# Kernel optimization log

Measured on AMD Instinct MI355X. Metric: run time of the kernel, lower is better.

Reference implementation:

```python
import jax, jax.numpy as jnp
import numpy as np

T = 5          # Newton-Schulz iterations
EPS = 1e-05


def reference(X):
    # X: (B, C, L); training-mode IterNorm whitening with num_groups=1
    B, C, L = X.shape
    x = jnp.transpose(X, (1, 0, 2)).reshape(C, -1)        # (d, m)
    d, m = x.shape
    mean = jnp.mean(x, axis=-1, keepdims=True)
    xc = x - mean                                         # (d, m)
    I = jnp.eye(d, dtype=X.dtype)
    Sigma = I * EPS + (xc @ xc.T) * (1.0 / m)             # (d, d)
    rTr = 1.0 / jnp.trace(Sigma)                          # scalar
    Sigma_N = Sigma * rTr
    P = I
    for _ in range(T):
        P = 1.5 * P - 0.5 * (P @ P @ P) @ Sigma_N
    wm = P * jnp.sqrt(rTr)                                # whitening matrix
    xn = wm @ xc                                          # (d, m)
    Xn = jnp.transpose(xn.reshape(C, B, L), (1, 0, 2))
    return Xn


def setup_inputs() -> dict:
    key = jax.random.key(0)
    X = jax.random.normal(key, (32, 64, 8192), dtype=jnp.float32)
    return {"X": X}
```

## Files before the change

### kernel.cpp

```cpp
#include <hip/hip_runtime.h>
#include <math.h>

#define L_DIM   8192
#define NCH     64
#define M_TOT_F 262144.0f
#define EPS_F   1e-5f
#define GTPB    4
#define ATPB    4
#define PSTRIDE 4224

typedef float f32x4 __attribute__((ext_vector_type(4)));
typedef short bf16x8 __attribute__((ext_vector_type(8)));

union U8 { unsigned u[4]; bf16x8 v; };

__device__ __forceinline__ void cvt2(float f0, float f1, unsigned& h, unsigned& l) {
    unsigned u0 = __float_as_uint(f0), u1 = __float_as_uint(f1);
    h = (u0 >> 16) | (u1 & 0xFFFF0000u);
    float r0 = f0 - __uint_as_float(u0 & 0xFFFF0000u);
    float r1 = f1 - __uint_as_float(u1 & 0xFFFF0000u);
    l = (__float_as_uint(r0) >> 16) | (__float_as_uint(r1) & 0xFFFF0000u);
}

__device__ __forceinline__ void split16(float v, unsigned short& h, unsigned short& l) {
    unsigned u = __float_as_uint(v);
    h = (unsigned short)(u >> 16);
    float r = v - __uint_as_float(u & 0xFFFF0000u);
    l = (unsigned short)(__float_as_uint(r) >> 16);
}

__device__ __forceinline__ f32x4 mfma16(bf16x8 a, bf16x8 b, f32x4 c) {
    return __builtin_amdgcn_mfma_f32_16x16x32_bf16(a, b, c, 0, 0, 0);
}

__device__ __forceinline__ f32x4 fzero() {
    f32x4 z; z[0] = 0.f; z[1] = 0.f; z[2] = 0.f; z[3] = 0.f; return z;
}

__global__ __launch_bounds__(256) void gram_kernel(const float* __restrict__ X,
                                                   float* __restrict__ P) {
    __shared__ __align__(16) unsigned char arena[32768];
    unsigned short (*hfrag)[4096] = (unsigned short(*)[4096])(arena);
    unsigned short (*lfrag)[4096] = (unsigned short(*)[4096])(arena + 16384);
    float* fg2 = (float*)arena;

    const int tid  = threadIdx.x;
    const int w    = tid >> 6;
    const int lane = tid & 63;
    const int m    = lane & 15;
    const int q    = lane >> 4;
    const int row  = 16 * w + m;

    f32x4 acc1[4], acc2[4];
#pragma unroll
    for (int nb = 0; nb < 4; ++nb) { acc1[nb] = fzero(); acc2[nb] = fzero(); }
    float sacc = 0.f;

    const int tile0 = blockIdx.x * GTPB;
    float4 v[GTPB][4];
#pragma unroll
    for (int t = 0; t < GTPB; ++t) {
        int tt = tile0 + t;
        const float* src = X + ((size_t)((tt >> 7) * NCH + row)) * L_DIM + ((tt & 127) << 6) + 8 * q;
        v[t][0] = *(const float4*)(src);
        v[t][1] = *(const float4*)(src + 4);
        v[t][2] = *(const float4*)(src + 32);
        v[t][3] = *(const float4*)(src + 36);
    }

#pragma unroll
    for (int t = 0; t < GTPB; ++t) {
        const int p = t & 1;
#pragma unroll
        for (int i = 0; i < 4; ++i) sacc += v[t][i].x + v[t][i].y + v[t][i].z + v[t][i].w;

        bf16x8 Ah[2], Al[2];
#pragma unroll
        for (int k = 0; k < 2; ++k) {
            U8 H, L;
            cvt2(v[t][2 * k].x,     v[t][2 * k].y,     H.u[0], L.u[0]);
            cvt2(v[t][2 * k].z,     v[t][2 * k].w,     H.u[1], L.u[1]);
            cvt2(v[t][2 * k + 1].x, v[t][2 * k + 1].y, H.u[2], L.u[2]);
            cvt2(v[t][2 * k + 1].z, v[t][2 * k + 1].w, H.u[3], L.u[3]);
            Ah[k] = H.v; Al[k] = L.v;
            int chunk = ((w * 2 + k) * 4 + q) * 16 + m;
            *(bf16x8*)&hfrag[p][chunk * 8] = H.v;
            *(bf16x8*)&lfrag[p][chunk * 8] = L.v;
        }
        __syncthreads();

#pragma unroll
        for (int k = 0; k < 2; ++k)
#pragma unroll
            for (int nb = 0; nb < 4; ++nb) {
                int chunk = ((nb * 2 + k) * 4 + q) * 16 + m;
                bf16x8 bh = *(const bf16x8*)&hfrag[p][chunk * 8];
                bf16x8 bl = *(const bf16x8*)&lfrag[p][chunk * 8];
                acc1[nb] = mfma16(Ah[k], bh, acc1[nb]);
                acc2[nb] = mfma16(Ah[k], bl, acc2[nb]);
            }
    }

    __syncthreads();
#pragma unroll
    for (int nb = 0; nb < 4; ++nb)
#pragma unroll
        for (int r = 0; r < 4; ++r) {
            int grow = 16 * w + 4 * q + r;
            int gcol = 16 * nb + m;
            fg2[grow * 65 + gcol] = acc2[nb][r];
        }
    __syncthreads();

    float* base = P + (size_t)blockIdx.x * PSTRIDE;
#pragma unroll
    for (int nb = 0; nb < 4; ++nb)
#pragma unroll
        for (int r = 0; r < 4; ++r) {
            int grow = 16 * w + 4 * q + r;
            int gcol = 16 * nb + m;
            base[grow * 64 + gcol] = acc1[nb][r] + acc2[nb][r] + fg2[gcol * 65 + grow];
        }
    sacc += __shfl_xor(sacc, 16);
    sacc += __shfl_xor(sacc, 32);
    if (q == 0) base[4096 + row] = sacc;
}

__global__ __launch_bounds__(256) void reduce_kernel(const float* __restrict__ P,
                                                     float* __restrict__ H0,
                                                     float* __restrict__ H1) {
    const int tid = threadIdx.x;
    const int w = tid >> 6, lane = tid & 63;
    const int s = blockIdx.x % 65;
    const int h = blockIdx.x / 65;
    const int e0 = s * 64;
    const float* base = P + (size_t)(h * 512 + w * 128) * PSTRIDE + e0 + lane;
    float a0 = 0.f, a1 = 0.f, a2 = 0.f, a3 = 0.f;
#pragma unroll 8
    for (int i = 0; i < 32; ++i) {
        const float* p = base + (size_t)(4 * i) * PSTRIDE;
        a0 += p[0];
        a1 += p[PSTRIDE];
        a2 += p[2 * PSTRIDE];
        a3 += p[3 * PSTRIDE];
    }
    float a = (a0 + a1) + (a2 + a3);
    __shared__ float red[4][64];
    red[w][lane] = a;
    __syncthreads();
    if (w == 0) {
        float r = red[0][lane] + red[1][lane] + red[2][lane] + red[3][lane];
        (h ? H1 : H0)[e0 + lane] = r;
    }
}

__device__ __forceinline__ void mm_core8(f32x4* acc,
                                         const unsigned short* Xh, const unsigned short* Xl,
                                         const unsigned short* Yh, const unsigned short* Yl,
                                         int rg, int nbb, int m, int q) {
#pragma unroll
    for (int k0 = 0; k0 < 64; k0 += 32) {
        bf16x8 xh = *(const bf16x8*)&Xh[(16 * rg + m) * 72 + k0 + 8 * q];
        bf16x8 xl = *(const bf16x8*)&Xl[(16 * rg + m) * 72 + k0 + 8 * q];
#pragma unroll
        for (int j = 0; j < 2; ++j) {
            int nb = nbb + j;
            bf16x8 yh = *(const bf16x8*)&Yh[(16 * nb + m) * 72 + k0 + 8 * q];
            bf16x8 yl = *(const bf16x8*)&Yl[(16 * nb + m) * 72 + k0 + 8 * q];
            acc[j] = mfma16(xh, yh, acc[j]);
            acc[j] = mfma16(xh, yl, acc[j]);
            acc[j] = mfma16(xl, yh, acc[j]);
        }
    }
}

__device__ __forceinline__ void mm_pl8(unsigned short* Dh, unsigned short* Dl,
                                       const unsigned short* Xh, const unsigned short* Xl,
                                       const unsigned short* Yh, const unsigned short* Yl,
                                       int rg, int nbb, int m, int q) {
    f32x4 acc[2];
    acc[0] = fzero(); acc[1] = fzero();
    mm_core8(acc, Xh, Xl, Yh, Yl, rg, nbb, m, q);
#pragma unroll
    for (int j = 0; j < 2; ++j)
#pragma unroll
        for (int r = 0; r < 4; ++r) {
            int row = 16 * rg + 4 * q + r, col = 16 * (nbb + j) + m;
            unsigned short h, l;
            split16(acc[j][r], h, l);
            Dh[row * 72 + col] = h;
            Dl[row * 72 + col] = l;
        }
}

__global__ __launch_bounds__(512) void ns_kernel(float* __restrict__ ws,
                                                 const float* __restrict__ H1) {
    __shared__ __align__(16) float Pf[64 * 68];
    __shared__ __align__(16) unsigned short Ph[64 * 72], Pl[64 * 72];
    __shared__ __align__(16) unsigned short Sh[64 * 72], Sl[64 * 72];
    __shared__ __align__(16) unsigned short T1h[64 * 72], T1l[64 * 72];
    __shared__ __align__(16) unsigned short T2h[64 * 72], T2l[64 * 72];
    __shared__ float mu[64];
    __shared__ float scal[2];

    const int tid = threadIdx.x;
    const int w8 = tid >> 6, lane = tid & 63;
    const int m = lane & 15, q = lane >> 4;
    const int rg = w8 >> 1, nbb = (w8 & 1) << 1;
    const float inv_m = 1.0f / M_TOT_F;

    if (tid < 64) mu[tid] = (ws[4096 + tid] + H1[4096 + tid]) * inv_m;
    __syncthreads();

    if (tid < 64) {
        int e = tid * 65;
        float g  = (ws[e] + H1[e]) * inv_m;
        float sd = g - mu[tid] * mu[tid] + EPS_F;
#pragma unroll
        for (int off = 32; off >= 1; off >>= 1) sd += __shfl_xor(sd, off);
        if (tid == 0) { scal[0] = 1.0f / sd; scal[1] = sqrtf(1.0f / sd); }
    }
    __syncthreads();
    const float rTr = scal[0];

    for (int e = tid; e < 4096; e += 512) {
        int i = e >> 6, j = e & 63;
        float g   = (ws[e] + H1[e]) * inv_m;
        float sig = g - mu[i] * mu[j] + ((i == j) ? EPS_F : 0.f);
        float sn  = sig * rTr;
        unsigned short h, l;
        split16(sn, h, l);
        Sh[i * 72 + j] = h; Sl[i * 72 + j] = l;
        float pv = ((i == j) ? 1.5f : 0.f) - 0.5f * sn;
        Pf[i * 68 + j] = pv;
        split16(pv, h, l);
        Ph[i * 72 + j] = h; Pl[i * 72 + j] = l;
    }
    __syncthreads();

    for (int it = 0; it < 4; ++it) {
        mm_pl8(T1h, T1l, Ph, Pl, Ph, Pl, rg, nbb, m, q);
        __syncthreads();
        mm_pl8(T2h, T2l, T1h, T1l, Ph, Pl, rg, nbb, m, q);
        __syncthreads();
        f32x4 acc[2];
        acc[0] = fzero(); acc[1] = fzero();
        mm_core8(acc, T2h, T2l, Sh, Sl, rg, nbb, m, q);
#pragma unroll
        for (int j = 0; j < 2; ++j)
#pragma unroll
            for (int r = 0; r < 4; ++r) {
                int row = 16 * rg + 4 * q + r, col = 16 * (nbb + j) + m;
                int idx = row * 68 + col;
                float pv = 1.5f * Pf[idx] - 0.5f * acc[j][r];
                Pf[idx] = pv;
                unsigned short h, l;
                split16(pv, h, l);
                Ph[row * 72 + col] = h;
                Pl[row * 72 + col] = l;
            }
        __syncthreads();
    }

    const float s = scal[1];
    unsigned short* hp = (unsigned short*)ws;
    unsigned short* lp = hp + 4096;
    for (int e = tid; e < 4096; e += 512) {
        int i = e >> 6, j = e & 63;
        float v = Pf[i * 68 + j] * s;
        unsigned short h, l;
        split16(v, h, l);
        hp[e] = h;
        lp[e] = l;
    }
    if (tid < 64) {
        float a = 0.f;
#pragma unroll 8
        for (int k = 0; k < 64; ++k) a += Pf[tid * 68 + k] * mu[k];
        ws[8256 + tid] = -a * s;
    }
}

__global__ __launch_bounds__(256) void apply_kernel(const float* __restrict__ X,
                                                    float* __restrict__ Y,
                                                    const float* __restrict__ ws) {
    __shared__ __align__(16) unsigned short hplane[2][4096];
    __shared__ __align__(16) unsigned short lplane[2][4096];
    const int tid  = threadIdx.x;
    const int w    = tid >> 6;
    const int lane = tid & 63;
    const int m    = lane & 15;
    const int q    = lane >> 4;
    const int cp   = tid & 31;
    const int lg   = tid >> 5;

    const unsigned short* hp = (const unsigned short*)ws;
    const unsigned short* lp = hp + 4096;
    bf16x8 Ah[2], Al[2];
#pragma unroll
    for (int kk = 0; kk < 2; ++kk) {
        Ah[kk] = *(const bf16x8*)&hp[(16 * w + m) * 64 + 32 * kk + 8 * q];
        Al[kk] = *(const bf16x8*)&lp[(16 * w + m) * 64 + 32 * kk + 8 * q];
    }
    const float4 bias4 = *(const float4*)&ws[8256 + 16 * w + 4 * q];

    float4 va[ATPB][2], vb[ATPB][2];
#pragma unroll
    for (int t = 0; t < ATPB; ++t) {
        int tile = blockIdx.x * ATPB + t;
        const float* xb = X + (size_t)(tile >> 7) * (NCH * L_DIM) + ((tile & 127) << 6)
                          + (size_t)(2 * cp) * L_DIM + 4 * lg;
#pragma unroll
        for (int ss = 0; ss < 2; ++ss) {
            va[t][ss] = *(const float4*)(xb + 32 * ss);
            vb[t][ss] = *(const float4*)(xb + 32 * ss + L_DIM);
        }
    }

#pragma unroll
    for (int t = 0; t < ATPB; ++t) {
        int tile = blockIdx.x * ATPB + t;
        int bidx = tile >> 7;
        int l0   = (tile & 127) << 6;
        const int p = t & 1;
        unsigned* hw2 = (unsigned*)hplane[p];
        unsigned* lw2 = (unsigned*)lplane[p];

#pragma unroll
        for (int ss = 0; ss < 2; ++ss) {
            float fa[4], fb[4];
            *(float4*)fa = va[t][ss];
            *(float4*)fb = vb[t][ss];
#pragma unroll
            for (int i = 0; i < 4; ++i) {
                int l = 4 * lg + 32 * ss + i;
                unsigned h, lo2;
                cvt2(fa[i], fb[i], h, lo2);
                int widx = l * 32 + (((cp >> 2) ^ (l & 7)) << 2) + (cp & 3);
                hw2[widx] = h;
                lw2[widx] = lo2;
            }
        }
        __syncthreads();

        f32x4 acc[4];
#pragma unroll
        for (int nb = 0; nb < 4; ++nb) {
            acc[nb][0] = bias4.x; acc[nb][1] = bias4.y;
            acc[nb][2] = bias4.z; acc[nb][3] = bias4.w;
        }
#pragma unroll
        for (int kk = 0; kk < 2; ++kk)
#pragma unroll
            for (int nb = 0; nb < 4; ++nb) {
                int l = 16 * nb + m;
                int saddr = l * 64 + ((((4 * kk + q) ^ (l & 7))) << 3);
                bf16x8 bh = *(const bf16x8*)&hplane[p][saddr];
                bf16x8 bl = *(const bf16x8*)&lplane[p][saddr];
                acc[nb] = mfma16(Ah[kk], bh, acc[nb]);
                acc[nb] = mfma16(Ah[kk], bl, acc[nb]);
                acc[nb] = mfma16(Al[kk], bh, acc[nb]);
            }

#pragma unroll
        for (int nb = 0; nb < 4; ++nb)
#pragma unroll
            for (int rr = 0; rr < 4; ++rr)
                Y[((size_t)bidx * NCH + 16 * w + 4 * q + rr) * L_DIM + l0 + 16 * nb + m] = acc[nb][rr];
    }
}

extern "C" void kernel_launch(void* const* d_in, const int* in_sizes, int n_in,
                              void* d_out, int out_size, void* d_ws, size_t ws_size,
                              hipStream_t stream) {
    const float* X = (const float*)d_in[0];
    float* Y  = (float*)d_out;
    float* ws = (float*)d_ws;
    float* scratch = (float*)d_out;
    float* H1 = scratch + (size_t)1024 * PSTRIDE;

    hipLaunchKernelGGL(gram_kernel,   dim3(1024), dim3(256), 0, stream, X, scratch);
    hipLaunchKernelGGL(reduce_kernel, dim3(130),  dim3(256), 0, stream, scratch, ws, H1);
    hipLaunchKernelGGL(ns_kernel,     dim3(1),    dim3(512), 0, stream, ws, H1);
    hipLaunchKernelGGL(apply_kernel,  dim3(1024), dim3(256), 0, stream, X, Y, ws);
}
```

Before: 147.0 us.

## Fuse partial-Gram reduction with Newton-Schulz via last-block-done election

Merges the reduce kernel and the single-block Newton-Schulz kernel into one launch. Each of 130 blocks reduces its slice of the partial Gram buffers and writes it to workspace with atomic stores. A global atomic counter then elects the last finishing block to run the Newton-Schulz iterations, reading the reduced sums through agent-scope atomic loads. This removes one kernel launch and its gap, at the cost of a global counter and fences, and the elected block starts only after all others finish.

```diff
diff --git a/kernel.cpp b/kernel.cpp
--- a/kernel.cpp
+++ b/kernel.cpp
@@ -8,11 +8,15 @@
 #define GTPB    4
 #define ATPB    4
 #define PSTRIDE 4224
+#define WSH     8448
+#define HSTR    4224
 
 typedef float f32x4 __attribute__((ext_vector_type(4)));
 typedef short bf16x8 __attribute__((ext_vector_type(8)));
 
 union U8 { unsigned u[4]; bf16x8 v; };
+
+__device__ unsigned rns_count;
 
 __device__ __forceinline__ void cvt2(float f0, float f1, unsigned& h, unsigned& l) {
     unsigned u0 = __float_as_uint(f0), u1 = __float_as_uint(f1);
@@ -27,6 +31,10 @@
     h = (unsigned short)(u >> 16);
     float r = v - __uint_as_float(u & 0xFFFF0000u);
     l = (unsigned short)(__float_as_uint(r) >> 16);
+}
+
+__device__ __forceinline__ float aload(const float* p) {
+    return __hip_atomic_load(p, __ATOMIC_RELAXED, __HIP_MEMORY_SCOPE_AGENT);
 }
 
 __device__ __forceinline__ f32x4 mfma16(bf16x8 a, bf16x8 b, f32x4 c) {
@@ -126,34 +134,6 @@
     if (q == 0) base[4096 + row] = sacc;
 }
 
-__global__ __launch_bounds__(256) void reduce_kernel(const float* __restrict__ P,
-                                                     float* __restrict__ H0,
-                                                     float* __restrict__ H1) {
-    const int tid = threadIdx.x;
-    const int w = tid >> 6, lane = tid & 63;
-    const int s = blockIdx.x % 65;
-    const int h = blockIdx.x / 65;
-    const int e0 = s * 64;
-    const float* base = P + (size_t)(h * 512 + w * 128) * PSTRIDE + e0 + lane;
-    float a0 = 0.f, a1 = 0.f, a2 = 0.f, a3 = 0.f;
-#pragma unroll 8
-    for (int i = 0; i < 32; ++i) {
-        const float* p = base + (size_t)(4 * i) * PSTRIDE;
-        a0 += p[0];
-        a1 += p[PSTRIDE];
-        a2 += p[2 * PSTRIDE];
-        a3 += p[3 * PSTRIDE];
-    }
-    float a = (a0 + a1) + (a2 + a3);
-    __shared__ float red[4][64];
-    red[w][lane] = a;
-    __syncthreads();
-    if (w == 0) {
-        float r = red[0][lane] + red[1][lane] + red[2][lane] + red[3][lane];
-        (h ? H1 : H0)[e0 + lane] = r;
-    }
-}
-
 __device__ __forceinline__ void mm_core8(f32x4* acc,
                                          const unsigned short* Xh, const unsigned short* Xl,
                                          const unsigned short* Yh, const unsigned short* Yl,
@@ -193,8 +173,8 @@
         }
 }
 
-__global__ __launch_bounds__(512) void ns_kernel(float* __restrict__ ws,
-                                                 const float* __restrict__ H1) {
+__global__ __launch_bounds__(512) void reduce_ns_kernel(const float* __restrict__ P,
+                                                        float* __restrict__ ws) {
     __shared__ __align__(16) float Pf[64 * 68];
     __shared__ __align__(16) unsigned short Ph[64 * 72], Pl[64 * 72];
     __shared__ __align__(16) unsigned short Sh[64 * 72], Sl[64 * 72];
@@ -202,6 +182,8 @@
     __shared__ __align__(16) unsigned short T2h[64 * 72], T2l[64 * 72];
     __shared__ float mu[64];
     __shared__ float scal[2];
+    __shared__ float red[8][64];
+    __shared__ unsigned elect;
 
     const int tid = threadIdx.x;
     const int w8 = tid >> 6, lane = tid & 63;
@@ -209,12 +191,48 @@
     const int rg = w8 >> 1, nbb = (w8 & 1) << 1;
     const float inv_m = 1.0f / M_TOT_F;
 
-    if (tid < 64) mu[tid] = (ws[4096 + tid] + H1[4096 + tid]) * inv_m;
+    {
+        const int s = blockIdx.x % 65;
+        const int h = blockIdx.x / 65;
+        const int e0 = s * 64;
+        const float* base = P + (size_t)(h * 512 + w8 * 64) * PSTRIDE + e0 + lane;
+        float a0 = 0.f, a1 = 0.f, a2 = 0.f, a3 = 0.f;
+#pragma unroll 4
+        for (int i = 0; i < 16; ++i) {
+            const float* p = base + (size_t)(4 * i) * PSTRIDE;
+            a0 += p[0];
+            a1 += p[PSTRIDE];
+            a2 += p[2 * PSTRIDE];
+            a3 += p[3 * PSTRIDE];
+        }
+        red[w8][lane] = (a0 + a1) + (a2 + a3);
+        __syncthreads();
+        if (w8 == 0) {
+            float r = ((red[0][lane] + red[1][lane]) + (red[2][lane] + red[3][lane]))
+                    + ((red[4][lane] + red[5][lane]) + (red[6][lane] + red[7][lane]));
+            __hip_atomic_store(&ws[WSH + h * HSTR + e0 + lane], r,
+                               __ATOMIC_RELAXED, __HIP_MEMORY_SCOPE_AGENT);
+        }
+    }
+    __syncthreads();
+    if (tid == 0) {
+        __threadfence();
+        unsigned o = __hip_atomic_fetch_add(&rns_count, 1u, __ATOMIC_ACQ_REL,
+                                            __HIP_MEMORY_SCOPE_AGENT);
+        elect = (o == 129) ? 1u : 0u;
+        if (o == 129)
+            __hip_atomic_store(&rns_count, 0u, __ATOMIC_RELAXED, __HIP_MEMORY_SCOPE_AGENT);
+    }
+    __syncthreads();
+    if (!elect) return;
+    __threadfence();
+
+    if (tid < 64) mu[tid] = (aload(&ws[WSH + 4096 + tid]) + aload(&ws[WSH + HSTR + 4096 + tid])) * inv_m;
     __syncthreads();
 
     if (tid < 64) {
         int e = tid * 65;
-        float g  = (ws[e] + H1[e]) * inv_m;
+        float g  = (aload(&ws[WSH + e]) + aload(&ws[WSH + HSTR + e])) * inv_m;
         float sd = g - mu[tid] * mu[tid] + EPS_F;
 #pragma unroll
         for (int off = 32; off >= 1; off >>= 1) sd += __shfl_xor(sd, off);
@@ -225,7 +243,7 @@
 
     for (int e = tid; e < 4096; e += 512) {
         int i = e >> 6, j = e & 63;
-        float g   = (ws[e] + H1[e]) * inv_m;
+        float g   = (aload(&ws[WSH + e]) + aload(&ws[WSH + HSTR + e])) * inv_m;
         float sig = g - mu[i] * mu[j] + ((i == j) ? EPS_F : 0.f);
         float sn  = sig * rTr;
         unsigned short h, l;
@@ -377,10 +395,8 @@
     float* Y  = (float*)d_out;
     float* ws = (float*)d_ws;
     float* scratch = (float*)d_out;
-    float* H1 = scratch + (size_t)1024 * PSTRIDE;
-
-    hipLaunchKernelGGL(gram_kernel,   dim3(1024), dim3(256), 0, stream, X, scratch);
-    hipLaunchKernelGGL(reduce_kernel, dim3(130),  dim3(256), 0, stream, scratch, ws, H1);
-    hipLaunchKernelGGL(ns_kernel,     dim3(1),    dim3(512), 0, stream, ws, H1);
-    hipLaunchKernelGGL(apply_kernel,  dim3(1024), dim3(256), 0, stream, X, Y, ws);
-}
+
+    hipLaunchKernelGGL(gram_kernel,      dim3(1024), dim3(256), 0, stream, X, scratch);
+    hipLaunchKernelGGL(reduce_ns_kernel, dim3(130),  dim3(512), 0, stream, scratch, ws);
+    hipLaunchKernelGGL(apply_kernel,     dim3(1024), dim3(256), 0, stream, X, Y, ws);
+}
```

Measured after the change: 150.6 us. 1.02x slower.

## Stream gram tile loads through 3-slot ring, widen NS kernel to 16 waves

Applied to the files above, without the earlier changes.

The gram kernel now keeps only three tiles of loaded input in registers and issues the fourth tile's load after the first tile is converted, instead of loading all four up front. Together with a min-blocks-per-CU launch bound on the gram and apply kernels, this lowers register pressure so more blocks can be resident. The single-block Newton-Schulz kernel moves from 8 to 16 waves, each computing one 16x16 output tile instead of two, to shorten the serial critical path of that one block. The risks are that the register cap forces spills, and that the smaller per-wave work in the NS kernel leaves more of its time in synchronisation.

```diff
diff --git a/kernel.cpp b/kernel.cpp
--- a/kernel.cpp
+++ b/kernel.cpp
@@ -37,8 +37,8 @@
     f32x4 z; z[0] = 0.f; z[1] = 0.f; z[2] = 0.f; z[3] = 0.f; return z;
 }
 
-__global__ __launch_bounds__(256) void gram_kernel(const float* __restrict__ X,
-                                                   float* __restrict__ P) {
+__global__ __launch_bounds__(256, 4) void gram_kernel(const float* __restrict__ X,
+                                                      float* __restrict__ P) {
     __shared__ __align__(16) unsigned char arena[32768];
     unsigned short (*hfrag)[4096] = (unsigned short(*)[4096])(arena);
     unsigned short (*lfrag)[4096] = (unsigned short(*)[4096])(arena + 16384);
@@ -57,36 +57,43 @@
     float sacc = 0.f;
 
     const int tile0 = blockIdx.x * GTPB;
-    float4 v[GTPB][4];
+    float4 v[3][4];
+
+#define LDT(slot, tt)  {                                                                   \
+        const float* src_ = X + ((size_t)(((tt) >> 7) * NCH + row)) * L_DIM                \
+                              + (((tt) & 127) << 6) + 8 * q;                               \
+        v[slot][0] = *(const float4*)(src_);                                               \
+        v[slot][1] = *(const float4*)(src_ + 4);                                           \
+        v[slot][2] = *(const float4*)(src_ + 32);                                          \
+        v[slot][3] = *(const float4*)(src_ + 36);                                          \
+    }
+
+#pragma unroll
+    for (int t = 0; t < 3; ++t) LDT(t, tile0 + t)
+
 #pragma unroll
     for (int t = 0; t < GTPB; ++t) {
-        int tt = tile0 + t;
-        const float* src = X + ((size_t)((tt >> 7) * NCH + row)) * L_DIM + ((tt & 127) << 6) + 8 * q;
-        v[t][0] = *(const float4*)(src);
-        v[t][1] = *(const float4*)(src + 4);
-        v[t][2] = *(const float4*)(src + 32);
-        v[t][3] = *(const float4*)(src + 36);
-    }
-
-#pragma unroll
-    for (int t = 0; t < GTPB; ++t) {
-        const int p = t & 1;
-#pragma unroll
-        for (int i = 0; i < 4; ++i) sacc += v[t][i].x + v[t][i].y + v[t][i].z + v[t][i].w;
+        const int slot = t % 3;
+        const int p    = t & 1;
+#pragma unroll
+        for (int i = 0; i < 4; ++i)
+            sacc += v[slot][i].x + v[slot][i].y + v[slot][i].z + v[slot][i].w;
 
         bf16x8 Ah[2], Al[2];
 #pragma unroll
         for (int k = 0; k < 2; ++k) {
             U8 H, L;
-            cvt2(v[t][2 * k].x,     v[t][2 * k].y,     H.u[0], L.u[0]);
-            cvt2(v[t][2 * k].z,     v[t][2 * k].w,     H.u[1], L.u[1]);
-            cvt2(v[t][2 * k + 1].x, v[t][2 * k + 1].y, H.u[2], L.u[2]);
-            cvt2(v[t][2 * k + 1].z, v[t][2 * k + 1].w, H.u[3], L.u[3]);
+            cvt2(v[slot][2 * k].x,     v[slot][2 * k].y,     H.u[0], L.u[0]);
+            cvt2(v[slot][2 * k].z,     v[slot][2 * k].w,     H.u[1], L.u[1]);
+            cvt2(v[slot][2 * k + 1].x, v[slot][2 * k + 1].y, H.u[2], L.u[2]);
+            cvt2(v[slot][2 * k + 1].z, v[slot][2 * k + 1].w, H.u[3], L.u[3]);
             Ah[k] = H.v; Al[k] = L.v;
             int chunk = ((w * 2 + k) * 4 + q) * 16 + m;
             *(bf16x8*)&hfrag[p][chunk * 8] = H.v;
             *(bf16x8*)&lfrag[p][chunk * 8] = L.v;
         }
+
+        if (t + 3 < GTPB) LDT(slot, tile0 + t + 3)
         __syncthreads();
 
 #pragma unroll
@@ -100,6 +107,7 @@
                 acc2[nb] = mfma16(Ah[k], bl, acc2[nb]);
             }
     }
+#undef LDT
 
     __syncthreads();
 #pragma unroll
@@ -154,47 +162,40 @@
     }
 }
 
-__device__ __forceinline__ void mm_core8(f32x4* acc,
-                                         const unsigned short* Xh, const unsigned short* Xl,
-                                         const unsigned short* Yh, const unsigned short* Yl,
-                                         int rg, int nbb, int m, int q) {
+__device__ __forceinline__ void mm_core16(f32x4& acc,
+                                          const unsigned short* Xh, const unsigned short* Xl,
+                                          const unsigned short* Yh, const unsigned short* Yl,
+                                          int rg, int nb, int m, int q) {
 #pragma unroll
     for (int k0 = 0; k0 < 64; k0 += 32) {
         bf16x8 xh = *(const bf16x8*)&Xh[(16 * rg + m) * 72 + k0 + 8 * q];
         bf16x8 xl = *(const bf16x8*)&Xl[(16 * rg + m) * 72 + k0 + 8 * q];
-#pragma unroll
-        for (int j = 0; j < 2; ++j) {
-            int nb = nbb + j;
-            bf16x8 yh = *(const bf16x8*)&Yh[(16 * nb + m) * 72 + k0 + 8 * q];
-            bf16x8 yl = *(const bf16x8*)&Yl[(16 * nb + m) * 72 + k0 + 8 * q];
-            acc[j] = mfma16(xh, yh, acc[j]);
-            acc[j] = mfma16(xh, yl, acc[j]);
-            acc[j] = mfma16(xl, yh, acc[j]);
-        }
-    }
-}
-
-__device__ __forceinline__ void mm_pl8(unsigned short* Dh, unsigned short* Dl,
-                                       const unsigned short* Xh, const unsigned short* Xl,
-                                       const unsigned short* Yh, const unsigned short* Yl,
-                                       int rg, int nbb, int m, int q) {
-    f32x4 acc[2];
-    acc[0] = fzero(); acc[1] = fzero();
-    mm_core8(acc, Xh, Xl, Yh, Yl, rg, nbb, m, q);
-#pragma unroll
-    for (int j = 0; j < 2; ++j)
-#pragma unroll
-        for (int r = 0; r < 4; ++r) {
-            int row = 16 * rg + 4 * q + r, col = 16 * (nbb + j) + m;
-            unsigned short h, l;
-            split16(acc[j][r], h, l);
-            Dh[row * 72 + col] = h;
-            Dl[row * 72 + col] = l;
-        }
-}
-
-__global__ __launch_bounds__(512) void ns_kernel(float* __restrict__ ws,
-                                                 const float* __restrict__ H1) {
+        bf16x8 yh = *(const bf16x8*)&Yh[(16 * nb + m) * 72 + k0 + 8 * q];
+        bf16x8 yl = *(const bf16x8*)&Yl[(16 * nb + m) * 72 + k0 + 8 * q];
+        acc = mfma16(xh, yh, acc);
+        acc = mfma16(xh, yl, acc);
+        acc = mfma16(xl, yh, acc);
+    }
+}
+
+__device__ __forceinline__ void mm_pl16(unsigned short* Dh, unsigned short* Dl,
+                                        const unsigned short* Xh, const unsigned short* Xl,
+                                        const unsigned short* Yh, const unsigned short* Yl,
+                                        int rg, int nb, int m, int q) {
+    f32x4 acc = fzero();
+    mm_core16(acc, Xh, Xl, Yh, Yl, rg, nb, m, q);
+#pragma unroll
+    for (int r = 0; r < 4; ++r) {
+        int row = 16 * rg + 4 * q + r, col = 16 * nb + m;
+        unsigned short h, l;
+        split16(acc[r], h, l);
+        Dh[row * 72 + col] = h;
+        Dl[row * 72 + col] = l;
+    }
+}
+
+__global__ __launch_bounds__(1024) void ns_kernel(float* __restrict__ ws,
+                                                  const float* __restrict__ H1) {
     __shared__ __align__(16) float Pf[64 * 68];
     __shared__ __align__(16) unsigned short Ph[64 * 72], Pl[64 * 72];
     __shared__ __align__(16) unsigned short Sh[64 * 72], Sl[64 * 72];
@@ -204,9 +205,9 @@
     __shared__ float scal[2];
 
     const int tid = threadIdx.x;
-    const int w8 = tid >> 6, lane = tid & 63;
+    const int w16 = tid >> 6, lane = tid & 63;
     const int m = lane & 15, q = lane >> 4;
-    const int rg = w8 >> 1, nbb = (w8 & 1) << 1;
+    const int rg = w16 >> 2, nb = w16 & 3;
     const float inv_m = 1.0f / M_TOT_F;
 
     if (tid < 64) mu[tid] = (ws[4096 + tid] + H1[4096 + tid]) * inv_m;
@@ -223,7 +224,7 @@
     __syncthreads();
     const float rTr = scal[0];
 
-    for (int e = tid; e < 4096; e += 512) {
+    for (int e = tid; e < 4096; e += 1024) {
         int i = e >> 6, j = e & 63;
         float g   = (ws[e] + H1[e]) * inv_m;
         float sig = g - mu[i] * mu[j] + ((i == j) ? EPS_F : 0.f);
@@ -239,33 +240,30 @@
     __syncthreads();
 
     for (int it = 0; it < 4; ++it) {
-        mm_pl8(T1h, T1l, Ph, Pl, Ph, Pl, rg, nbb, m, q);
-        __syncthreads();
-        mm_pl8(T2h, T2l, T1h, T1l, Ph, Pl, rg, nbb, m, q);
-        __syncthreads();
-        f32x4 acc[2];
-        acc[0] = fzero(); acc[1] = fzero();
-        mm_core8(acc, T2h, T2l, Sh, Sl, rg, nbb, m, q);
-#pragma unroll
-        for (int j = 0; j < 2; ++j)
-#pragma unroll
-            for (int r = 0; r < 4; ++r) {
-                int row = 16 * rg + 4 * q + r, col = 16 * (nbb + j) + m;
-                int idx = row * 68 + col;
-                float pv = 1.5f * Pf[idx] - 0.5f * acc[j][r];
-                Pf[idx] = pv;
-                unsigned short h, l;
-                split16(pv, h, l);
-                Ph[row * 72 + col] = h;
-                Pl[row * 72 + col] = l;
-            }
+        mm_pl16(T1h, T1l, Ph, Pl, Ph, Pl, rg, nb, m, q);
+        __syncthreads();
+        mm_pl16(T2h, T2l, T1h, T1l, Ph, Pl, rg, nb, m, q);
+        __syncthreads();
+        f32x4 acc = fzero();
+        mm_core16(acc, T2h, T2l, Sh, Sl, rg, nb, m, q);
+#pragma unroll
+        for (int r = 0; r < 4; ++r) {
+            int row = 16 * rg + 4 * q + r, col = 16 * nb + m;
+            int idx = row * 68 + col;
+            float pv = 1.5f * Pf[idx] - 0.5f * acc[r];
+            Pf[idx] = pv;
+            unsigned short h, l;
+            split16(pv, h, l);
+            Ph[row * 72 + col] = h;
+            Pl[row * 72 + col] = l;
+        }
         __syncthreads();
     }
 
     const float s = scal[1];
     unsigned short* hp = (unsigned short*)ws;
     unsigned short* lp = hp + 4096;
-    for (int e = tid; e < 4096; e += 512) {
+    for (int e = tid; e < 4096; e += 1024) {
         int i = e >> 6, j = e & 63;
         float v = Pf[i * 68 + j] * s;
         unsigned short h, l;
@@ -281,9 +279,9 @@
     }
 }
 
-__global__ __launch_bounds__(256) void apply_kernel(const float* __restrict__ X,
-                                                    float* __restrict__ Y,
-                                                    const float* __restrict__ ws) {
+__global__ __launch_bounds__(256, 4) void apply_kernel(const float* __restrict__ X,
+                                                       float* __restrict__ Y,
+                                                       const float* __restrict__ ws) {
     __shared__ __align__(16) unsigned short hplane[2][4096];
     __shared__ __align__(16) unsigned short lplane[2][4096];
     const int tid  = threadIdx.x;
@@ -379,8 +377,8 @@
     float* scratch = (float*)d_out;
     float* H1 = scratch + (size_t)1024 * PSTRIDE;
 
-    hipLaunchKernelGGL(gram_kernel,   dim3(1024), dim3(256), 0, stream, X, scratch);
-    hipLaunchKernelGGL(reduce_kernel, dim3(130),  dim3(256), 0, stream, scratch, ws, H1);
-    hipLaunchKernelGGL(ns_kernel,     dim3(1),    dim3(512), 0, stream, ws, H1);
-    hipLaunchKernelGGL(apply_kernel,  dim3(1024), dim3(256), 0, stream, X, Y, ws);
-}
+    hipLaunchKernelGGL(gram_kernel,   dim3(1024), dim3(256),  0, stream, X, scratch);
+    hipLaunchKernelGGL(reduce_kernel, dim3(130),  dim3(256),  0, stream, scratch, ws, H1);
+    hipLaunchKernelGGL(ns_kernel,     dim3(1),    dim3(1024), 0, stream, ws, H1);
+    hipLaunchKernelGGL(apply_kernel,  dim3(1024), dim3(256),  0, stream, X, Y, ws);
+}
```

After: 150.2 us. 2.2% more time.
